# Optimization experiments

Hardware: AMD Instinct MI355X
Metric: run time of the kernel (lower is better)

The kernel has to match this reference:

```python
import jax, jax.numpy as jnp
import numpy as np

V, E, H, LM, LC = 50257, 512, 1024, 128, 256


def gru_cell(x, h, Wih, Whh, bih, bhh):
    # PyTorch nn.GRU cell, gate order (r, z, n)
    gi = x @ Wih.T + bih
    gh = h @ Whh.T + bhh
    i_r, i_z, i_n = jnp.split(gi, 3, -1)
    h_r, h_z, h_n = jnp.split(gh, 3, -1)
    r = jax.nn.sigmoid(i_r + h_r)
    z = jax.nn.sigmoid(i_z + h_z)
    n = jnp.tanh(i_n + r * h_n)
    return (1.0 - z) * n + z * h


def setup_inputs() -> dict:
    key = jax.random.key(0)
    ks = jax.random.split(key, 18)
    f = lambda k, sh: jax.random.normal(k, sh, jnp.float32) * 0.02
    return {
        "motion": jax.random.randint(ks[0], (1, LM), 0, V),
        "target_output": jax.random.randint(ks[1], (1, LC), 0, V),
        "enc_emb": f(ks[2], (V, E)),
        "enc_Wih": f(ks[3], (3 * H, E)),
        "enc_Whh": f(ks[4], (3 * H, H)),
        "enc_bih": f(ks[5], (3 * H,)),
        "enc_bhh": f(ks[6], (3 * H,)),
        "dec_emb": f(ks[7], (V, H)),
        "dec_Wih": f(ks[8], (3 * H, H)),
        "dec_Whh": f(ks[9], (3 * H, H)),
        "dec_bih": f(ks[10], (3 * H,)),
        "dec_bhh": f(ks[11], (3 * H,)),
        "attn_W": f(ks[12], (LM, 2 * H)),
        "attn_b": f(ks[13], (LM,)),
        "comb_W": f(ks[14], (H, 2 * H)),
        "comb_b": f(ks[15], (H,)),
        "out_W": f(ks[16], (V, H)),
        "out_b": f(ks[17], (V,)),
    }


def reference(motion, target_output, enc_emb, enc_Wih, enc_Whh, enc_bih, enc_bhh,
              dec_emb, dec_Wih, dec_Whh, dec_bih, dec_bhh,
              attn_W, attn_b, comb_W, comb_b, out_W, out_b):
    # ----- encode: per-step GRU over motion tokens (batch is hard-coded 1) -----
    toks = motion[0]  # [LM]

    def enc_step(h, t):
        h2 = gru_cell(enc_emb[t], h, enc_Wih, enc_Whh, enc_bih, enc_bhh)
        return h2, h2

    h0 = jnp.zeros((H,), jnp.float32)
    enc_h, enc_outs = jax.lax.scan(enc_step, h0, toks)  # enc_outs: [LM, H]

    # ----- decode with teacher forcing -----
    # original: decoder_input = SOS at idx 0, then target[idx-1] set at end of
    # step idx => step idx+1 consumes target[idx-1]; step 1 consumes target[-1].
    tgt = target_output[0]  # [LC]
    dec_in = jnp.concatenate([jnp.zeros((1,), tgt.dtype), tgt[-1:], tgt[:-2]])  # [LC]

    def dec_step(h, t):
        emb = dec_emb[t]  # [H] (dropout is identity at inference)
        attn_w = jax.nn.softmax(jnp.concatenate([emb, h]) @ attn_W.T + attn_b)  # [LM]
        ctx = attn_w @ enc_outs  # [H]
        x = jnp.concatenate([emb, ctx]) @ comb_W.T + comb_b  # [H] (no relu in source)
        h2 = gru_cell(x, h, dec_Wih, dec_Whh, dec_bih, dec_bhh)
        logp = jax.nn.log_softmax(h2 @ out_W.T + out_b)  # [V]
        return h2, logp

    _, logps = jax.lax.scan(dec_step, enc_h, dec_in)  # [LC, V]
    return logps[None]  # [1, LC, V] (permute(1,0,2) with batch=1)
```

## Files before the change

### kernel.cpp

```cpp
#include <hip/hip_runtime.h>

#define V_ 50257
#define E_ 512
#define H_ 1024
#define LM_ 128
#define LC_ 256
#define NBLK 256
#define ROWS 12
#define AREP 16
#define NT_OUT 786

typedef __attribute__((ext_vector_type(8))) short short8;
typedef __attribute__((ext_vector_type(4))) float f32x4;
typedef unsigned long long u64;

__device__ __forceinline__ unsigned short f2bf(float x) {
  union { float f; unsigned u; } v; v.f = x;
  unsigned r = v.u + 0x7fffu + ((v.u >> 16) & 1u);
  return (unsigned short)(r >> 16);
}
__device__ __forceinline__ float bflo(unsigned u) { union { unsigned u; float f; } v; v.u = u << 16; return v.f; }
__device__ __forceinline__ float bfhi(unsigned u) { union { unsigned u; float f; } v; v.u = u & 0xffff0000u; return v.f; }

__device__ __forceinline__ int grow4(int s, int i0) {
  return (s < 4) ? (i0 + s) : (s < 8) ? (1024 + i0 + (s - 4)) : (2048 + i0 + (s - 8));
}

__device__ __forceinline__ void st_u32(unsigned* p, unsigned v) {
  __hip_atomic_store(p, v, __ATOMIC_RELAXED, __HIP_MEMORY_SCOPE_AGENT);
}
__device__ __forceinline__ void st_u64(u64* p, u64 v) {
  __hip_atomic_store(p, v, __ATOMIC_RELAXED, __HIP_MEMORY_SCOPE_AGENT);
}
__device__ __forceinline__ u64 ld_u64(const u64* p) {
  return __hip_atomic_load(p, __ATOMIC_RELAXED, __HIP_MEMORY_SCOPE_AGENT);
}
__device__ __forceinline__ unsigned ld_u32(const unsigned* p) {
  return __hip_atomic_load(p, __ATOMIC_RELAXED, __HIP_MEMORY_SCOPE_AGENT);
}
__device__ __forceinline__ void atom_add_f32(float* p, float v) {
  (void)__hip_atomic_fetch_add(p, v, __ATOMIC_RELAXED, __HIP_MEMORY_SCOPE_AGENT);
}

__global__ void build_dec_tok(const int* __restrict__ tgt, int* __restrict__ dtok) {
  int t = threadIdx.x;
  dtok[t] = (t == 0) ? 0 : (t == 1 ? tgt[LC_ - 1] : tgt[t - 2]);
}

__global__ __launch_bounds__(256) void gemm_g(const float* __restrict__ A, int lda,
                                              const int* __restrict__ ridx,
                                              const float* __restrict__ B, int ldb,
                                              const float* __restrict__ bias,
                                              float* __restrict__ C, int ldc, int K) {
  __shared__ float As[16][68];
  __shared__ float Bs[16][68];
  const int bm = blockIdx.y * 64, bn = blockIdx.x * 64;
  const int tid = threadIdx.x;
  const int tx = tid & 15, ty = tid >> 4;
  const int lm = tid & 63, lk = (tid >> 6) * 4;
  const int arow = ridx ? ridx[bm + lm] : (bm + lm);
  const float* Arow = A + (size_t)arow * lda;
  float acc[4][4] = {};
  for (int k0 = 0; k0 < K; k0 += 16) {
    float4 av = *(const float4*)&Arow[k0 + lk];
    float4 bv = *(const float4*)&B[(size_t)(bn + lm) * ldb + k0 + lk];
    As[lk + 0][lm] = av.x; As[lk + 1][lm] = av.y; As[lk + 2][lm] = av.z; As[lk + 3][lm] = av.w;
    Bs[lk + 0][lm] = bv.x; Bs[lk + 1][lm] = bv.y; Bs[lk + 2][lm] = bv.z; Bs[lk + 3][lm] = bv.w;
    __syncthreads();
#pragma unroll
    for (int kk = 0; kk < 16; ++kk) {
      float4 a4 = *(const float4*)&As[kk][ty * 4];
      float4 b4 = *(const float4*)&Bs[kk][tx * 4];
      acc[0][0] += a4.x * b4.x; acc[0][1] += a4.x * b4.y; acc[0][2] += a4.x * b4.z; acc[0][3] += a4.x * b4.w;
      acc[1][0] += a4.y * b4.x; acc[1][1] += a4.y * b4.y; acc[1][2] += a4.y * b4.z; acc[1][3] += a4.y * b4.w;
      acc[2][0] += a4.z * b4.x; acc[2][1] += a4.z * b4.y; acc[2][2] += a4.z * b4.z; acc[2][3] += a4.z * b4.w;
      acc[3][0] += a4.w * b4.x; acc[3][1] += a4.w * b4.y; acc[3][2] += a4.w * b4.z; acc[3][3] += a4.w * b4.w;
    }
    __syncthreads();
  }
#pragma unroll
  for (int i = 0; i < 4; ++i) {
#pragma unroll
    for (int j = 0; j < 4; ++j) {
      int gm = bm + ty * 4 + i, gn = bn + tx * 4 + j;
      float bv = bias ? bias[gn] : 0.f;
      C[(size_t)gm * ldc + gn] = acc[i][j] + bv;
    }
  }
}

__global__ __launch_bounds__(256) void gemm_dual(const float* __restrict__ A, int lda,
                                                 const int* __restrict__ ridx,
                                                 const float* __restrict__ combW,
                                                 const float* __restrict__ comb_b,
                                                 const float* __restrict__ attnW,
                                                 const float* __restrict__ attn_b,
                                                 float* __restrict__ xE,
                                                 float* __restrict__ aE, int K) {
  __shared__ float As[16][68];
  __shared__ float Bs[16][68];
  const int bm = blockIdx.y * 64;
  const bool is_x = blockIdx.x < 16;
  const int bn = (is_x ? blockIdx.x : (blockIdx.x - 16)) * 64;
  const float* B = is_x ? combW : attnW;
  const int ldb = 2048;
  const float* bias = is_x ? comb_b : attn_b;
  float* C = is_x ? xE : aE;
  const int ldc = is_x ? 1024 : 128;
  const int tid = threadIdx.x;
  const int tx = tid & 15, ty = tid >> 4;
  const int lm = tid & 63, lk = (tid >> 6) * 4;
  const int arow = ridx[bm + lm];
  const float* Arow = A + (size_t)arow * lda;
  float acc[4][4] = {};
  for (int k0 = 0; k0 < K; k0 += 16) {
    float4 av = *(const float4*)&Arow[k0 + lk];
    float4 bv = *(const float4*)&B[(size_t)(bn + lm) * ldb + k0 + lk];
    As[lk + 0][lm] = av.x; As[lk + 1][lm] = av.y; As[lk + 2][lm] = av.z; As[lk + 3][lm] = av.w;
    Bs[lk + 0][lm] = bv.x; Bs[lk + 1][lm] = bv.y; Bs[lk + 2][lm] = bv.z; Bs[lk + 3][lm] = bv.w;
    __syncthreads();
#pragma unroll
    for (int kk = 0; kk < 16; ++kk) {
      float4 a4 = *(const float4*)&As[kk][ty * 4];
      float4 b4 = *(const float4*)&Bs[kk][tx * 4];
      acc[0][0] += a4.x * b4.x; acc[0][1] += a4.x * b4.y; acc[0][2] += a4.x * b4.z; acc[0][3] += a4.x * b4.w;
      acc[1][0] += a4.y * b4.x; acc[1][1] += a4.y * b4.y; acc[1][2] += a4.y * b4.z; acc[1][3] += a4.y * b4.w;
      acc[2][0] += a4.z * b4.x; acc[2][1] += a4.z * b4.y; acc[2][2] += a4.z * b4.z; acc[2][3] += a4.z * b4.w;
      acc[3][0] += a4.w * b4.x; acc[3][1] += a4.w * b4.y; acc[3][2] += a4.w * b4.z; acc[3][3] += a4.w * b4.w;
    }
    __syncthreads();
  }
#pragma unroll
  for (int i = 0; i < 4; ++i) {
#pragma unroll
    for (int j = 0; j < 4; ++j) {
      int gm = bm + ty * 4 + i, gn = bn + tx * 4 + j;
      C[(size_t)gm * ldc + gn] = acc[i][j] + bias[gn];
    }
  }
}

__global__ __launch_bounds__(256) void enc_rnn(const float* __restrict__ Whh,
                                               const float* __restrict__ bhh,
                                               const float* __restrict__ gi,
                                               u64* __restrict__ epk,
                                               float* __restrict__ outs) {
  __shared__ unsigned short Whl[ROWS][1024];
  __shared__ unsigned h_sh[512];
  __shared__ float h_own[4];
  __shared__ float bh[ROWS];
  __shared__ float ghl[ROWS];
  const int b = blockIdx.x, tid = threadIdx.x;
  const int w = tid >> 6, l = tid & 63;
  const int i0 = b * 4;
  for (int idx = tid; idx < ROWS * 1024; idx += 256) {
    int s = idx >> 10, c = idx & 1023;
    Whl[s][c] = f2bf(Whh[(size_t)grow4(s, i0) * H_ + c]);
  }
  if (tid < ROWS) bh[tid] = bhh[grow4(tid, i0)];
  if (tid < 4) h_own[tid] = 0.f;
  __syncthreads();

  for (int t = 0; t < LM_; ++t) {
    float gr = 0.f, gz = 0.f, gn_ = 0.f;
    if (tid < 4) {
      const float* git = gi + (size_t)t * 3072;
      gr = git[i0 + tid]; gz = git[1024 + i0 + tid]; gn_ = git[2048 + i0 + tid];
    }
    if (t == 0) {
      h_sh[2 * tid] = 0u; h_sh[2 * tid + 1] = 0u;
    } else {
      const u64* pb = epk + (size_t)(t & 1) * 512 + 2 * tid;
      const unsigned g = (unsigned)t;
      u64 q0, q1;
      for (;;) {
        q0 = ld_u64(pb); q1 = ld_u64(pb + 1);
        if ((unsigned)(q0 >> 32) == g && (unsigned)(q1 >> 32) == g) break;
        __builtin_amdgcn_s_sleep(1);
      }
      h_sh[2 * tid] = (unsigned)q0;
      h_sh[2 * tid + 1] = (unsigned)q1;
    }
    __syncthreads();

    for (int s = w; s < ROWS; s += 4) {
      float acc = 0.f;
#pragma unroll
      for (int e = 0; e < 8; ++e) {
        unsigned u = *(const unsigned*)&Whl[s][2 * (e * 64 + l)];
        unsigned hv = h_sh[e * 64 + l];
        acc += bflo(u) * bflo(hv) + bfhi(u) * bfhi(hv);
      }
#pragma unroll
      for (int off = 32; off; off >>= 1) acc += __shfl_xor(acc, off);
      if (l == 0) ghl[s] = acc;
    }
    __syncthreads();
    if (tid < 4) {
      int i = tid, ig = i0 + i;
      float hr = ghl[i] + bh[i], hz = ghl[4 + i] + bh[4 + i], hn = ghl[8 + i] + bh[8 + i];
      float r = 1.f / (1.f + expf(-(gr + hr)));
      float z = 1.f / (1.f + expf(-(gz + hz)));
      float n = tanhf(gn_ + r * hn);
      float hpv = (1.f - z) * n + z * h_own[i];
      h_own[i] = hpv;
      float v0 = __shfl(hpv, 0), v1 = __shfl(hpv, 1);
      float v2 = __shfl(hpv, 2), v3 = __shfl(hpv, 3);
      if (tid == 0) {
        u64 gg = (u64)(unsigned)(t + 1) << 32;
        u64* pb = epk + (size_t)((t + 1) & 1) * 512 + 2 * b;
        st_u64(pb,     gg | (u64)((unsigned)f2bf(v0) | ((unsigned)f2bf(v1) << 16)));
        st_u64(pb + 1, gg | (u64)((unsigned)f2bf(v2) | ((unsigned)f2bf(v3) << 16)));
      }
      outs[(size_t)t * H_ + ig] = hpv;
    }
  }
}

__global__ __launch_bounds__(256) void dec_rnn(const float* __restrict__ Whh,
                                               const float* __restrict__ bhh,
                                               const float* __restrict__ attn_W,
                                               const float* __restrict__ G,
                                               const float* __restrict__ P1,
                                               const float* __restrict__ aE,
                                               const float* __restrict__ hfin,
                                               float* __restrict__ a_acc,
                                               u64* __restrict__ dpk,
                                               unsigned* __restrict__ dflags,
                                               unsigned short* __restrict__ Hs) {
  __shared__ unsigned short Whl[ROWS][1024];
  __shared__ unsigned Ac[2 * 128];
  __shared__ float Gl[ROWS][128];
  __shared__ unsigned h_sh[512];
  __shared__ float a_f[128];
  __shared__ float h_own[4];
  __shared__ float bh[ROWS];
  __shared__ float ghl[ROWS];
  __shared__ float giS[ROWS];
  const int b = blockIdx.x, tid = threadIdx.x;
  const int w = tid >> 6, l = tid & 63;
  const int i0 = b * 4;
  for (int idx = tid; idx < ROWS * 1024; idx += 256) {
    int s = idx >> 10, c = idx & 1023;
    Whl[s][c] = f2bf(Whh[(size_t)grow4(s, i0) * H_ + c]);
  }
  if (tid < 256) {
    int u = tid >> 7, j = tid & 127;
    float2 wv = *(const float2*)&attn_W[(size_t)j * 2048 + 1024 + i0 + 2 * u];
    Ac[tid] = (unsigned)f2bf(wv.x) | ((unsigned)f2bf(wv.y) << 16);
  }
  for (int idx = tid; idx < ROWS * 128; idx += 256) {
    int s = idx >> 7, c = idx & 127;
    Gl[s][c] = G[(size_t)grow4(s, i0) * 128 + c];
  }
  if (tid < ROWS) bh[tid] = bhh[grow4(tid, i0)];
  if (tid < 4) h_own[tid] = hfin[i0 + tid];
  __syncthreads();

  {
    float h0 = h_own[0], h1 = h_own[1], h2 = h_own[2], h3 = h_own[3];
    if (tid < 128) {
      unsigned w0 = Ac[tid], w1 = Ac[128 + tid];
      float a0 = bflo(w0) * h0 + bfhi(w0) * h1 + bflo(w1) * h2 + bfhi(w1) * h3;
      atom_add_f32(&a_acc[(b & (AREP - 1)) * 128 + tid], a0);
    }
    __syncthreads();
    if (tid == 0) st_u32(&dflags[b * 16], 1u);
  }

  for (int t = 0; t < LC_; ++t) {
    u64 aacc[16]; u64 aEv = 0;
    if (tid < 64) {
      const unsigned need = (unsigned)(t + 1);
      for (;;) {
        unsigned f0 = ld_u32(&dflags[tid * 16]);
        unsigned f1 = ld_u32(&dflags[(tid + 64) * 16]);
        unsigned f2 = ld_u32(&dflags[(tid + 128) * 16]);
        unsigned f3 = ld_u32(&dflags[(tid + 192) * 16]);
        unsigned mn = min(min(f0, f1), min(f2, f3));
        if (__all((int)(mn >= need))) break;
        __builtin_amdgcn_s_sleep(1);
      }
      const u64* ab = (const u64*)(a_acc + (size_t)t * (AREP * 128)) + l;
#pragma unroll
      for (int r = 0; r < AREP; ++r) aacc[r] = ld_u64(ab + r * 64);
      float2 ae2 = *(const float2*)&aE[(size_t)t * LM_ + 2 * l];
      aEv = ((u64)__float_as_uint(ae2.y) << 32) | (u64)__float_as_uint(ae2.x);
    }
    float p1p[3];
    if (l == 0) {
#pragma unroll
      for (int k = 0; k < 3; ++k) p1p[k] = P1[(size_t)t * 3072 + grow4(w + 4 * k, i0)];
    } else {
      p1p[0] = p1p[1] = p1p[2] = 0.f;
    }
    if (t == 0) {
      float4 hv = ((const float4*)hfin)[tid];
      h_sh[2 * tid] = (unsigned)f2bf(hv.x) | ((unsigned)f2bf(hv.y) << 16);
      h_sh[2 * tid + 1] = (unsigned)f2bf(hv.z) | ((unsigned)f2bf(hv.w) << 16);
    } else {
      const u64* pb = dpk + (size_t)(t & 1) * 512 + 2 * tid;
      const unsigned g = (unsigned)t;
      u64 q0, q1;
      for (;;) {
        q0 = ld_u64(pb); q1 = ld_u64(pb + 1);
        if ((unsigned)(q0 >> 32) == g && (unsigned)(q1 >> 32) == g) break;
        __builtin_amdgcn_s_sleep(1);
      }
      h_sh[2 * tid] = (unsigned)q0;
      h_sh[2 * tid + 1] = (unsigned)q1;
    }
    __syncthreads();

    if (tid < 64) {
      float s0 = 0.f, s1 = 0.f;
#pragma unroll
      for (int r = 0; r < AREP; ++r) {
        s0 += __uint_as_float((unsigned)aacc[r]);
        s1 += __uint_as_float((unsigned)(aacc[r] >> 32));
      }
      a_f[2 * l] = s0 + __uint_as_float((unsigned)aEv);
      a_f[2 * l + 1] = s1 + __uint_as_float((unsigned)(aEv >> 32));
    }
    for (int s = w; s < ROWS; s += 4) {
      float acc = 0.f;
#pragma unroll
      for (int e = 0; e < 8; ++e) {
        unsigned u = *(const unsigned*)&Whl[s][2 * (e * 64 + l)];
        unsigned hv = h_sh[e * 64 + l];
        acc += bflo(u) * bflo(hv) + bfhi(u) * bfhi(hv);
      }
#pragma unroll
      for (int off = 32; off; off >>= 1) acc += __shfl_xor(acc, off);
      if (l == 0) ghl[s] = acc;
    }
    __syncthreads();

    float ax = a_f[2 * l], ay = a_f[2 * l + 1];
    float mx = fmaxf(ax, ay);
#pragma unroll
    for (int off = 32; off; off >>= 1) mx = fmaxf(mx, __shfl_xor(mx, off));
    float pe0 = expf(ax - mx), pe1 = expf(ay - mx);
    float zs = pe0 + pe1;
#pragma unroll
    for (int off = 32; off; off >>= 1) zs += __shfl_xor(zs, off);
    float w0 = pe0 / zs, w1 = pe1 / zs;
#pragma unroll
    for (int k = 0; k < 3; ++k) {
      int s = w + 4 * k;
      float2 g2 = *(const float2*)&Gl[s][2 * l];
      float acc = g2.x * w0 + g2.y * w1;
#pragma unroll
      for (int off = 32; off; off >>= 1) acc += __shfl_xor(acc, off);
      if (l == 0) giS[s] = acc + p1p[k];
    }
    __syncthreads();

    if (tid < 4) {
      int i = tid, ig = i0 + i;
      float hr = ghl[i] + bh[i], hz = ghl[4 + i] + bh[4 + i], hn = ghl[8 + i] + bh[8 + i];
      float r = 1.f / (1.f + expf(-(giS[i] + hr)));
      float z = 1.f / (1.f + expf(-(giS[4 + i] + hz)));
      float n = tanhf(giS[8 + i] + r * hn);
      float hpv = (1.f - z) * n + z * h_own[i];
      h_own[i] = hpv;
      float v0 = __shfl(hpv, 0), v1 = __shfl(hpv, 1);
      float v2 = __shfl(hpv, 2), v3 = __shfl(hpv, 3);
      if (tid == 0 && t < LC_ - 1) {
        u64 gg = (u64)(unsigned)(t + 1) << 32;
        u64* pb = dpk + (size_t)((t + 1) & 1) * 512 + 2 * b;
        st_u64(pb,     gg | (u64)((unsigned)f2bf(v0) | ((unsigned)f2bf(v1) << 16)));
        st_u64(pb + 1, gg | (u64)((unsigned)f2bf(v2) | ((unsigned)f2bf(v3) << 16)));
      }
      Hs[(size_t)t * H_ + ig] = f2bf(hpv);
    }
    __syncthreads();

    if (t < LC_ - 1) {
      float h0 = h_own[0], h1 = h_own[1], h2 = h_own[2], h3 = h_own[3];
      if (tid < 128) {
        unsigned w0p = Ac[tid], w1p = Ac[128 + tid];
        float a0 = bflo(w0p) * h0 + bfhi(w0p) * h1 + bflo(w1p) * h2 + bfhi(w1p) * h3;
        atom_add_f32(&a_acc[(size_t)(t + 1) * (AREP * 128) + (b & (AREP - 1)) * 128 + tid], a0);
      }
    }
    __syncthreads();
    if (tid == 0) st_u32(&dflags[b * 16], (unsigned)(t + 2));
  }
}

__global__ __launch_bounds__(256) void out_gemm(const unsigned short* __restrict__ A,
                                                const float* __restrict__ Wf, int ldw,
                                                const float* __restrict__ bias,
                                                float* __restrict__ C,
                                                float* __restrict__ pmax,
                                                float* __restrict__ psum,
                                                int N, int K) {
  __shared__ unsigned short As[256][40];
  __shared__ unsigned short Bs[64][40];
  const int bn = blockIdx.x * 64, bx = blockIdx.x;
  const int tid = threadIdx.x, w = tid >> 6, l = tid & 63;
  f32x4 acc[4][4];
#pragma unroll
  for (int mf = 0; mf < 4; ++mf)
#pragma unroll
    for (int nf = 0; nf < 4; ++nf) acc[mf][nf] = (f32x4){0.f, 0.f, 0.f, 0.f};

  for (int k0 = 0; k0 < K; k0 += 32) {
    const unsigned short* src = A + (size_t)tid * K + k0;
#pragma unroll
    for (int kc = 0; kc < 4; ++kc) {
      short8 v = *(const short8*)(src + kc * 8);
      *(short8*)&As[tid][kc * 8] = v;
    }
#pragma unroll
    for (int c = 0; c < 2; ++c) {
      int idx = tid + c * 256;
      int n = idx >> 3, kc = idx & 7;
      int gn = bn + n;
      float4 v = {0.f, 0.f, 0.f, 0.f};
      if (gn < N) v = *(const float4*)&Wf[(size_t)gn * ldw + k0 + kc * 4];
      uint2 p;
      p.x = (unsigned)f2bf(v.x) | ((unsigned)f2bf(v.y) << 16);
      p.y = (unsigned)f2bf(v.z) | ((unsigned)f2bf(v.w) << 16);
      *(uint2*)&Bs[n][kc * 4] = p;
    }
    __syncthreads();
    const int k8 = (l >> 4) * 8;
    short8 af4[4], bf4[4];
#pragma unroll
    for (int mf = 0; mf < 4; ++mf) af4[mf] = *(const short8*)&As[w * 64 + mf * 16 + (l & 15)][k8];
#pragma unroll
    for (int nf = 0; nf < 4; ++nf) bf4[nf] = *(const short8*)&Bs[nf * 16 + (l & 15)][k8];
#pragma unroll
    for (int mf = 0; mf < 4; ++mf)
#pragma unroll
      for (int nf = 0; nf < 4; ++nf)
        acc[mf][nf] = __builtin_amdgcn_mfma_f32_16x16x32_bf16(af4[mf], bf4[nf], acc[mf][nf], 0, 0, 0);
    __syncthreads();
  }
#pragma unroll
  for (int mf = 0; mf < 4; ++mf) {
#pragma unroll
    for (int i = 0; i < 4; ++i) {
      int m = w * 64 + mf * 16 + (l >> 4) * 4 + i;
      float v[4];
#pragma unroll
      for (int nf = 0; nf < 4; ++nf) {
        int n = bn + nf * 16 + (l & 15);
        float val = -3.4e38f;
        if (n < N) {
          val = acc[mf][nf][i] + bias[n];
          C[(size_t)m * N + n] = val;
        }
        v[nf] = val;
      }
      float mv = fmaxf(fmaxf(v[0], v[1]), fmaxf(v[2], v[3]));
#pragma unroll
      for (int off = 1; off < 16; off <<= 1) mv = fmaxf(mv, __shfl_xor(mv, off));
      float se = 0.f;
#pragma unroll
      for (int nf = 0; nf < 4; ++nf) se += (v[nf] > -1e38f) ? expf(v[nf] - mv) : 0.f;
#pragma unroll
      for (int off = 1; off < 16; off <<= 1) se += __shfl_xor(se, off);
      if ((l & 15) == 0) {
        pmax[(size_t)m * NT_OUT + bx] = mv;
        psum[(size_t)m * NT_OUT + bx] = se;
      }
    }
  }
}

__global__ __launch_bounds__(256) void lsm_combine(const float* __restrict__ pmax,
                                                   const float* __restrict__ psum,
                                                   float* __restrict__ stats) {
  const int r = blockIdx.x, tid = threadIdx.x, w = tid >> 6, l = tid & 63;
  __shared__ float red[4];
  __shared__ float Msh;
  const float* pm = pmax + (size_t)r * NT_OUT;
  const float* ps = psum + (size_t)r * NT_OUT;
  float m = -3.4e38f;
  for (int j = tid; j < NT_OUT; j += 256) m = fmaxf(m, pm[j]);
#pragma unroll
  for (int off = 32; off; off >>= 1) m = fmaxf(m, __shfl_xor(m, off));
  if (l == 0) red[w] = m;
  __syncthreads();
  if (tid == 0) Msh = fmaxf(fmaxf(red[0], red[1]), fmaxf(red[2], red[3]));
  __syncthreads();
  float M = Msh;
  float s = 0.f;
  for (int j = tid; j < NT_OUT; j += 256) s += ps[j] * expf(pm[j] - M);
#pragma unroll
  for (int off = 32; off; off >>= 1) s += __shfl_xor(s, off);
  if (l == 0) red[w] = s;
  __syncthreads();
  if (tid == 0) {
    stats[r] = M;
    stats[256 + r] = logf(red[0] + red[1] + red[2] + red[3]);
  }
}

__global__ __launch_bounds__(256) void lsm_apply(float* __restrict__ C, const float* __restrict__ stats, int N) {
  int r = blockIdx.y;
  int ci = blockIdx.x * 256 + threadIdx.x;
  if (ci < N) {
    size_t idx = (size_t)r * N + ci;
    C[idx] = C[idx] - stats[r] - stats[256 + r];
  }
}

extern "C" void kernel_launch(void* const* d_in, const int* in_sizes, int n_in,
                              void* d_out, int out_size, void* d_ws, size_t ws_size,
                              hipStream_t stream) {
  (void)in_sizes; (void)n_in; (void)out_size; (void)ws_size;
  const int* motion = (const int*)d_in[0];
  const int* tgt = (const int*)d_in[1];
  const float* enc_emb = (const float*)d_in[2];
  const float* enc_Wih = (const float*)d_in[3];
  const float* enc_Whh = (const float*)d_in[4];
  const float* enc_bih = (const float*)d_in[5];
  const float* enc_bhh = (const float*)d_in[6];
  const float* dec_emb = (const float*)d_in[7];
  const float* dec_Wih = (const float*)d_in[8];
  const float* dec_Whh = (const float*)d_in[9];
  const float* dec_bih = (const float*)d_in[10];
  const float* dec_bhh = (const float*)d_in[11];
  const float* attn_W = (const float*)d_in[12];
  const float* attn_b = (const float*)d_in[13];
  const float* comb_W = (const float*)d_in[14];
  const float* comb_b = (const float*)d_in[15];
  const float* out_W = (const float*)d_in[16];
  const float* out_b = (const float*)d_in[17];
  float* out = (float*)d_out;

  float* wsf = (float*)d_ws;
  size_t o = 0;
  auto F = [&](size_t n) { float* p = wsf + o; o += (n + 3) & ~(size_t)3; return p; };
  float* enc_gi = F(128 * 3072);
  float* enc_outs = F(128 * 1024);
  float* aE = F(256 * 128);
  float* xE = F(256 * 1024);
  float* P1 = F(256 * 3072);
  float* M2T = F(128 * 1024);
  float* Gm = F(3072 * 128);
  int* dec_tok = (int*)F(256);
  u64* epk = (u64*)F(2048);
  u64* dpk = (u64*)F(2048);
  unsigned* dflags = (unsigned*)F(4096);
  float* a_acc = F(LC_ * AREP * 128);
  float* stats = F(512);
  float* pmax = F(256 * NT_OUT);
  float* psum = F(256 * NT_OUT);
  unsigned short* Hs = (unsigned short*)F(256 * 1024 / 2);

  hipMemsetAsync(epk, 0, (2048 + 2048 + 4096 + LC_ * AREP * 128) * sizeof(float), stream);

  build_dec_tok<<<1, 256, 0, stream>>>(tgt, dec_tok);
  gemm_g<<<dim3(48, 2), 256, 0, stream>>>(enc_emb, 512, motion, enc_Wih, 512, enc_bih, enc_gi, 3072, 512);
  gemm_dual<<<dim3(18, 4), 256, 0, stream>>>(dec_emb, 1024, dec_tok, comb_W, comb_b, attn_W, attn_b, xE, aE, 1024);
  gemm_g<<<dim3(48, 4), 256, 0, stream>>>(xE, 1024, nullptr, dec_Wih, 1024, dec_bih, P1, 3072, 1024);

  enc_rnn<<<NBLK, 256, 0, stream>>>(enc_Whh, enc_bhh, enc_gi, epk, enc_outs);

  gemm_g<<<dim3(16, 2), 256, 0, stream>>>(enc_outs, 1024, nullptr, comb_W + 1024, 2048, nullptr, M2T, 1024, 1024);
  gemm_g<<<dim3(2, 48), 256, 0, stream>>>(dec_Wih, 1024, nullptr, M2T, 1024, nullptr, Gm, 128, 1024);

  dec_rnn<<<NBLK, 256, 0, stream>>>(dec_Whh, dec_bhh, attn_W, Gm, P1, aE,
                                    enc_outs + (size_t)(LM_ - 1) * H_, a_acc, dpk, dflags, Hs);

  out_gemm<<<NT_OUT, 256, 0, stream>>>(Hs, out_W, 1024, out_b, out, pmax, psum, V_, 1024);
  lsm_combine<<<256, 256, 0, stream>>>(pmax, psum, stats);
  lsm_apply<<<dim3(197, 256), 256, 0, stream>>>(out, stats, V_);
}
```

Measured before the change: 2.349 ms.

## Double-buffer output GEMM tiles and remove a barrier from decoder step

The output-projection GEMM now uses two LDS buffers and register-prefetches the next K-slice of activations and weights while MFMAs run on the current slice, leaving one barrier per iteration instead of two. In the persistent decoder kernel, every thread computes the four GRU hidden updates redundantly from a register copy of h_own. The attention partial atomic-add and the flag publish are issued right after that, so one __syncthreads per timestep goes away. The cost is doubled shared memory in the GEMM and redundant transcendental math per thread in the decoder.

New measurement: 2.500 ms. 6.5% more time.

```diff
diff --git a/kernel.cpp b/kernel.cpp
--- a/kernel.cpp
+++ b/kernel.cpp
@@ -269,6 +269,7 @@
   }
 
   for (int t = 0; t < LC_; ++t) {
+    float hown0 = h_own[0], hown1 = h_own[1], hown2 = h_own[2], hown3 = h_own[3];
     u64 aacc[16]; u64 aEv = 0;
     if (tid < 64) {
       const unsigned need = (unsigned)(t + 1);
@@ -356,33 +357,32 @@
     }
     __syncthreads();
 
-    if (tid < 4) {
-      int i = tid, ig = i0 + i;
+    float hp[4];
+#pragma unroll
+    for (int i = 0; i < 4; ++i) {
+      float hold = (i == 0) ? hown0 : (i == 1) ? hown1 : (i == 2) ? hown2 : hown3;
       float hr = ghl[i] + bh[i], hz = ghl[4 + i] + bh[4 + i], hn = ghl[8 + i] + bh[8 + i];
       float r = 1.f / (1.f + expf(-(giS[i] + hr)));
       float z = 1.f / (1.f + expf(-(giS[4 + i] + hz)));
       float n = tanhf(giS[8 + i] + r * hn);
-      float hpv = (1.f - z) * n + z * h_own[i];
-      h_own[i] = hpv;
-      float v0 = __shfl(hpv, 0), v1 = __shfl(hpv, 1);
-      float v2 = __shfl(hpv, 2), v3 = __shfl(hpv, 3);
-      if (tid == 0 && t < LC_ - 1) {
+      hp[i] = (1.f - z) * n + z * hold;
+    }
+    if (t < LC_ - 1) {
+      if (tid < 128) {
+        unsigned w0p = Ac[tid], w1p = Ac[128 + tid];
+        float a0 = bflo(w0p) * hp[0] + bfhi(w0p) * hp[1] + bflo(w1p) * hp[2] + bfhi(w1p) * hp[3];
+        atom_add_f32(&a_acc[(size_t)(t + 1) * (AREP * 128) + (b & (AREP - 1)) * 128 + tid], a0);
+      }
+      if (tid == 0) {
         u64 gg = (u64)(unsigned)(t + 1) << 32;
         u64* pb = dpk + (size_t)((t + 1) & 1) * 512 + 2 * b;
-        st_u64(pb,     gg | (u64)((unsigned)f2bf(v0) | ((unsigned)f2bf(v1) << 16)));
-        st_u64(pb + 1, gg | (u64)((unsigned)f2bf(v2) | ((unsigned)f2bf(v3) << 16)));
-      }
-      Hs[(size_t)t * H_ + ig] = f2bf(hpv);
-    }
-    __syncthreads();
-
-    if (t < LC_ - 1) {
-      float h0 = h_own[0], h1 = h_own[1], h2 = h_own[2], h3 = h_own[3];
-      if (tid < 128) {
-        unsigned w0p = Ac[tid], w1p = Ac[128 + tid];
-        float a0 = bflo(w0p) * h0 + bfhi(w0p) * h1 + bflo(w1p) * h2 + bfhi(w1p) * h3;
-        atom_add_f32(&a_acc[(size_t)(t + 1) * (AREP * 128) + (b & (AREP - 1)) * 128 + tid], a0);
-      }
+        st_u64(pb,     gg | (u64)((unsigned)f2bf(hp[0]) | ((unsigned)f2bf(hp[1]) << 16)));
+        st_u64(pb + 1, gg | (u64)((unsigned)f2bf(hp[2]) | ((unsigned)f2bf(hp[3]) << 16)));
+      }
+    }
+    if (tid < 4) {
+      h_own[tid] = hp[tid];
+      Hs[(size_t)t * H_ + i0 + tid] = f2bf(hp[tid]);
     }
     __syncthreads();
     if (tid == 0) st_u32(&dflags[b * 16], (unsigned)(t + 2));
@@ -396,48 +396,75 @@
                                                 float* __restrict__ pmax,
                                                 float* __restrict__ psum,
                                                 int N, int K) {
-  __shared__ unsigned short As[256][40];
-  __shared__ unsigned short Bs[64][40];
+  __shared__ unsigned short As[2][256][40];
+  __shared__ unsigned short Bs[2][64][40];
   const int bn = blockIdx.x * 64, bx = blockIdx.x;
   const int tid = threadIdx.x, w = tid >> 6, l = tid & 63;
+  const int NIT = K / 32;
   f32x4 acc[4][4];
 #pragma unroll
   for (int mf = 0; mf < 4; ++mf)
 #pragma unroll
     for (int nf = 0; nf < 4; ++nf) acc[mf][nf] = (f32x4){0.f, 0.f, 0.f, 0.f};
 
-  for (int k0 = 0; k0 < K; k0 += 32) {
-    const unsigned short* src = A + (size_t)tid * K + k0;
-#pragma unroll
-    for (int kc = 0; kc < 4; ++kc) {
-      short8 v = *(const short8*)(src + kc * 8);
-      *(short8*)&As[tid][kc * 8] = v;
-    }
-#pragma unroll
-    for (int c = 0; c < 2; ++c) {
-      int idx = tid + c * 256;
-      int n = idx >> 3, kc = idx & 7;
-      int gn = bn + n;
-      float4 v = {0.f, 0.f, 0.f, 0.f};
-      if (gn < N) v = *(const float4*)&Wf[(size_t)gn * ldw + k0 + kc * 4];
-      uint2 p;
-      p.x = (unsigned)f2bf(v.x) | ((unsigned)f2bf(v.y) << 16);
-      p.y = (unsigned)f2bf(v.z) | ((unsigned)f2bf(v.w) << 16);
-      *(uint2*)&Bs[n][kc * 4] = p;
-    }
-    __syncthreads();
+  const int bidx = tid + 0, bn_r0 = (tid) >> 3, bkc0 = tid & 7;
+  const int bn_r1 = (tid + 256) >> 3, bkc1 = (tid + 256) & 7;
+  (void)bidx;
+
+  short8 ar[4];
+  float4 fv[2];
+  {
+    const unsigned short* src = A + (size_t)tid * K;
+#pragma unroll
+    for (int kc = 0; kc < 4; ++kc) ar[kc] = *(const short8*)(src + kc * 8);
+    int gn0 = bn + bn_r0, gn1 = bn + bn_r1;
+    fv[0] = (gn0 < N) ? *(const float4*)&Wf[(size_t)gn0 * ldw + bkc0 * 4] : (float4){0, 0, 0, 0};
+    fv[1] = (gn1 < N) ? *(const float4*)&Wf[(size_t)gn1 * ldw + bkc1 * 4] : (float4){0, 0, 0, 0};
+#pragma unroll
+    for (int kc = 0; kc < 4; ++kc) *(short8*)&As[0][tid][kc * 8] = ar[kc];
+    uint2 p0, p1;
+    p0.x = (unsigned)f2bf(fv[0].x) | ((unsigned)f2bf(fv[0].y) << 16);
+    p0.y = (unsigned)f2bf(fv[0].z) | ((unsigned)f2bf(fv[0].w) << 16);
+    p1.x = (unsigned)f2bf(fv[1].x) | ((unsigned)f2bf(fv[1].y) << 16);
+    p1.y = (unsigned)f2bf(fv[1].z) | ((unsigned)f2bf(fv[1].w) << 16);
+    *(uint2*)&Bs[0][bn_r0][bkc0 * 4] = p0;
+    *(uint2*)&Bs[0][bn_r1][bkc1 * 4] = p1;
+  }
+
+  for (int it = 0; it < NIT; ++it) {
+    const int cur = it & 1, nxt = cur ^ 1;
+    __syncthreads();
+    if (it + 1 < NIT) {
+      int k0n = (it + 1) * 32;
+      const unsigned short* src = A + (size_t)tid * K + k0n;
+#pragma unroll
+      for (int kc = 0; kc < 4; ++kc) ar[kc] = *(const short8*)(src + kc * 8);
+      int gn0 = bn + bn_r0, gn1 = bn + bn_r1;
+      fv[0] = (gn0 < N) ? *(const float4*)&Wf[(size_t)gn0 * ldw + k0n + bkc0 * 4] : (float4){0, 0, 0, 0};
+      fv[1] = (gn1 < N) ? *(const float4*)&Wf[(size_t)gn1 * ldw + k0n + bkc1 * 4] : (float4){0, 0, 0, 0};
+    }
     const int k8 = (l >> 4) * 8;
     short8 af4[4], bf4[4];
 #pragma unroll
-    for (int mf = 0; mf < 4; ++mf) af4[mf] = *(const short8*)&As[w * 64 + mf * 16 + (l & 15)][k8];
-#pragma unroll
-    for (int nf = 0; nf < 4; ++nf) bf4[nf] = *(const short8*)&Bs[nf * 16 + (l & 15)][k8];
+    for (int mf = 0; mf < 4; ++mf) af4[mf] = *(const short8*)&As[cur][w * 64 + mf * 16 + (l & 15)][k8];
+#pragma unroll
+    for (int nf = 0; nf < 4; ++nf) bf4[nf] = *(const short8*)&Bs[cur][nf * 16 + (l & 15)][k8];
 #pragma unroll
     for (int mf = 0; mf < 4; ++mf)
 #pragma unroll
       for (int nf = 0; nf < 4; ++nf)
         acc[mf][nf] = __builtin_amdgcn_mfma_f32_16x16x32_bf16(af4[mf], bf4[nf], acc[mf][nf], 0, 0, 0);
-    __syncthreads();
+    if (it + 1 < NIT) {
+#pragma unroll
+      for (int kc = 0; kc < 4; ++kc) *(short8*)&As[nxt][tid][kc * 8] = ar[kc];
+      uint2 p0, p1;
+      p0.x = (unsigned)f2bf(fv[0].x) | ((unsigned)f2bf(fv[0].y) << 16);
+      p0.y = (unsigned)f2bf(fv[0].z) | ((unsigned)f2bf(fv[0].w) << 16);
+      p1.x = (unsigned)f2bf(fv[1].x) | ((unsigned)f2bf(fv[1].y) << 16);
+      p1.y = (unsigned)f2bf(fv[1].z) | ((unsigned)f2bf(fv[1].w) << 16);
+      *(uint2*)&Bs[nxt][bn_r0][bkc0 * 4] = p0;
+      *(uint2*)&Bs[nxt][bn_r1][bkc1 * 4] = p1;
+    }
   }
 #pragma unroll
   for (int mf = 0; mf < 4; ++mf) {
```
